# Kernel optimization log

Measured on AMD Instinct MI355X. Metric: run time of the kernel, lower is better.

## Reference

```python
import jax, jax.numpy as jnp
import numpy as np

B, T, IN, H = 4096, 128, 768, 256


def setup_inputs() -> dict:
    key = jax.random.key(0)
    ks = jax.random.split(key, 5)
    s1 = 1.0 / np.sqrt(IN)
    s2 = 1.0 / np.sqrt(H)
    return {
        "x": jax.random.normal(ks[0], (B, IN), jnp.float32),
        "W1": jax.random.normal(ks[1], (T, IN, H), jnp.float32) * s1,
        "b1": jnp.zeros((T, H), jnp.float32),
        "W2": jax.random.normal(ks[2], (T, H, H), jnp.float32) * s2,
        "b2": jnp.zeros((T, H), jnp.float32),
        "W3": jax.random.normal(ks[3], (T, H), jnp.float32) * s2,
        "b3": jnp.zeros((T,), jnp.float32),
    }


def reference(x, W1, b1, W2, b2, W3, b3):
    # Per-task 3-layer MLP, vectorized over tasks. Dropout is eval-mode (identity).
    h = jax.nn.relu(jnp.einsum('bi,tih->bth', x, W1) + b1)          # [B, T, H]
    h = jax.nn.relu(jnp.einsum('bth,thk->btk', h, W2) + b2)         # [B, T, H]
    out = jnp.einsum('bth,th->bt', h, W3) + b3                      # [B, T]
    return out
```

## Files before the change

kernel.cpp:

```cpp
#include <hip/hip_runtime.h>
#include <cstdint>
#include <cstddef>

#define B_   4096
#define T_   128
#define IN_  768
#define H_   256
#define BM_  256
#define KC1  (IN_ / 32)
#define KC2  (H_ / 32)

typedef __bf16 bf16_t;
typedef bf16_t bf16x8 __attribute__((ext_vector_type(8)));
typedef bf16_t bf16x4 __attribute__((ext_vector_type(4)));
typedef float  floatx16 __attribute__((ext_vector_type(16)));

#define MFMA32(a, b, c) __builtin_amdgcn_mfma_f32_32x32x16_bf16((a), (b), (c), 0, 0, 0)

__device__ __forceinline__ void gl_lds16(const bf16_t* g, bf16_t* l) {
    __builtin_amdgcn_global_load_lds(
        (const __attribute__((address_space(1))) void*)g,
        (__attribute__((address_space(3))) void*)l, 16, 0, 0);
}

__global__ __launch_bounds__(256)
void tile_w2(const float* __restrict__ src, bf16_t* __restrict__ dst, int K, int KC) {
    const int t  = blockIdx.x / KC;
    const int kc = blockIdx.x - t * KC;
    const int kq = threadIdx.x >> 6;
    const int h4 = (threadIdx.x & 63) * 4;
    const float* s = src + ((size_t)t * K + kc * 32 + kq * 8) * H_ + h4;
    float r[8][4];
#pragma unroll
    for (int e = 0; e < 8; ++e) {
        float4 v = *(const float4*)(s + (size_t)e * H_);
        r[e][0] = v.x; r[e][1] = v.y; r[e][2] = v.z; r[e][3] = v.w;
    }
    bf16_t* d = dst + (((size_t)(t * KC + kc) * 4 + kq) * H_ + h4) * 8;
#pragma unroll
    for (int c = 0; c < 4; ++c) {
        bf16x8 v;
#pragma unroll
        for (int e = 0; e < 8; ++e) v[e] = (bf16_t)r[e][c];
        *(bf16x8*)(d + c * 8) = v;
    }
}

__global__ void tile_x_kernel(const float* __restrict__ src, bf16_t* __restrict__ dst,
                              long long total8) {
    long long o = (long long)blockIdx.x * blockDim.x + threadIdx.x;
    if (o >= total8) return;
    int m = (int)(o & 127);
    long long q = o >> 7;
    int kq = (int)(q & 3);
    int q2 = (int)(q >> 2);
    int kc   = q2 % KC1;
    int mblk = q2 / KC1;
    const float* s = src + ((long long)mblk * 128 + m) * IN_ + kc * 32 + kq * 8;
    float4 a = *(const float4*)s;
    float4 b = *(const float4*)(s + 4);
    bf16x8 v;
    v[0] = (bf16_t)a.x; v[1] = (bf16_t)a.y; v[2] = (bf16_t)a.z; v[3] = (bf16_t)a.w;
    v[4] = (bf16_t)b.x; v[5] = (bf16_t)b.y; v[6] = (bf16_t)b.z; v[7] = (bf16_t)b.w;
    *(bf16x8*)(dst + o * 8) = v;
}

__global__ __launch_bounds__(512, 2)
void mtmlp_fused3(const bf16_t* __restrict__ xt, const bf16_t* __restrict__ w1t,
                  const float* __restrict__ b1, const bf16_t* __restrict__ w2t,
                  const float* __restrict__ b2, const float* __restrict__ W3,
                  const float* __restrict__ b3, float* __restrict__ out) {
    const int L    = blockIdx.x;
    const int xcd  = L & 7;
    const int slot = L >> 3;
    const int t    = xcd * 16 + (slot >> 4);
    const int mblk = slot & 15;
    const int m0   = mblk * BM_;
    const int mb0  = mblk * 2;

    const int tid  = threadIdx.x;
    const int lane = tid & 63;
    const int wid  = tid >> 6;
    const int wm   = wid >> 2;
    const int wn   = wid & 3;
    const int ln31 = lane & 31;
    const int hi   = lane >> 5;

    __shared__ __align__(16) bf16_t hbuf[BM_ * H_];
    __shared__ __align__(16) bf16_t wt2[4 * H_ * 8];
    float* w3s = (float*)wt2;

    floatx16 acc[4][2];
#pragma unroll
    for (int i = 0; i < 4; ++i)
#pragma unroll
        for (int j = 0; j < 2; ++j)
#pragma unroll
            for (int e = 0; e < 16; ++e) acc[i][j][e] = 0.0f;

    const bf16_t* w1base = w1t + (size_t)t * KC1 * 8192;
    const bf16_t* x0base = xt + (size_t)mb0 * KC1 * 4096;
    const bf16_t* x1base = xt + (size_t)(mb0 + 1) * KC1 * 4096;

    auto stage1 = [&](bf16_t* buf, int kc) {
        const bf16_t* ws = w1base + (size_t)kc * 8192;
        gl_lds16(ws + tid * 8,        buf + tid * 8);
        gl_lds16(ws + 4096 + tid * 8, buf + 4096 + tid * 8);
        gl_lds16(x0base + (size_t)kc * 4096 + tid * 8, buf + 8192 + tid * 8);
        gl_lds16(x1base + (size_t)kc * 4096 + tid * 8, buf + 12288 + tid * 8);
    };
    auto comp1 = [&](const bf16_t* buf) {
#pragma unroll
        for (int s = 0; s < 2; ++s) {
            const int kq = s * 2 + hi;
            bf16x8 A[4], Bf[2];
#pragma unroll
            for (int i = 0; i < 4; ++i)
                A[i] = *(const bf16x8*)(buf + (size_t)(kq * H_ + wm * 128 + i * 32 + ln31) * 8);
#pragma unroll
            for (int j = 0; j < 2; ++j) {
                const int mm = wn * 64 + j * 32 + ln31;
                Bf[j] = *(const bf16x8*)(buf + 8192 + (mm >> 7) * 4096 +
                                         (size_t)(kq * 128 + (mm & 127)) * 8);
            }
#pragma unroll
            for (int i = 0; i < 4; ++i)
#pragma unroll
                for (int j = 0; j < 2; ++j) acc[i][j] = MFMA32(A[i], Bf[j], acc[i][j]);
        }
    };

    bf16_t* buf0 = hbuf;
    bf16_t* buf1 = hbuf + 16384;
    stage1(buf0, 0);
    for (int kc = 0; kc < KC1; kc += 2) {
        __syncthreads();
        stage1(buf1, kc + 1);
        comp1(buf0);
        __syncthreads();
        if (kc + 2 < KC1) stage1(buf0, kc + 2);
        comp1(buf1);
    }
    __syncthreads();

#pragma unroll
    for (int i = 0; i < 4; ++i) {
#pragma unroll
        for (int g = 0; g < 4; ++g) {
            const int h0 = wm * 128 + i * 32 + g * 8 + 4 * hi;
            float4 bias = *(const float4*)(b1 + t * H_ + h0);
            const int blk = h0 >> 3;
#pragma unroll
            for (int j = 0; j < 2; ++j) {
                const int mm = wn * 64 + j * 32 + ln31;
                bf16x4 o;
                o[0] = (bf16_t)fmaxf(acc[i][j][4 * g + 0] + bias.x, 0.0f);
                o[1] = (bf16_t)fmaxf(acc[i][j][4 * g + 1] + bias.y, 0.0f);
                o[2] = (bf16_t)fmaxf(acc[i][j][4 * g + 2] + bias.z, 0.0f);
                o[3] = (bf16_t)fmaxf(acc[i][j][4 * g + 3] + bias.w, 0.0f);
                *(bf16x4*)(hbuf + (size_t)(blk * BM_ + mm) * 8 + 4 * hi) = o;
            }
        }
    }

#pragma unroll
    for (int i = 0; i < 4; ++i)
#pragma unroll
        for (int j = 0; j < 2; ++j)
#pragma unroll
            for (int e = 0; e < 16; ++e) acc[i][j][e] = 0.0f;

    const bf16_t* w2base = w2t + (size_t)t * KC2 * 8192;
    for (int kc = 0; kc < KC2; ++kc) {
        __syncthreads();
        const bf16_t* ws = w2base + (size_t)kc * 8192;
        gl_lds16(ws + tid * 8,        wt2 + tid * 8);
        gl_lds16(ws + 4096 + tid * 8, wt2 + 4096 + tid * 8);
        __syncthreads();
#pragma unroll
        for (int s = 0; s < 2; ++s) {
            const int kq = s * 2 + hi;
            bf16x8 A[4], Bf[2];
#pragma unroll
            for (int i = 0; i < 4; ++i)
                A[i] = *(const bf16x8*)(wt2 + (size_t)(kq * H_ + wm * 128 + i * 32 + ln31) * 8);
            const int blk = kc * 4 + kq;
#pragma unroll
            for (int j = 0; j < 2; ++j) {
                const int mm = wn * 64 + j * 32 + ln31;
                Bf[j] = *(const bf16x8*)(hbuf + (size_t)(blk * BM_ + mm) * 8);
            }
#pragma unroll
            for (int i = 0; i < 4; ++i)
#pragma unroll
                for (int j = 0; j < 2; ++j) acc[i][j] = MFMA32(A[i], Bf[j], acc[i][j]);
        }
    }

    __syncthreads();
    if (tid < H_) w3s[tid] = W3[t * H_ + tid];
#pragma unroll
    for (int i = 0; i < 4; ++i) {
#pragma unroll
        for (int g = 0; g < 4; ++g) {
            const int h0 = wm * 128 + i * 32 + g * 8 + 4 * hi;
            float4 bias = *(const float4*)(b2 + t * H_ + h0);
            const int blk = h0 >> 3;
#pragma unroll
            for (int j = 0; j < 2; ++j) {
                const int mm = wn * 64 + j * 32 + ln31;
                bf16x4 o;
                o[0] = (bf16_t)fmaxf(acc[i][j][4 * g + 0] + bias.x, 0.0f);
                o[1] = (bf16_t)fmaxf(acc[i][j][4 * g + 1] + bias.y, 0.0f);
                o[2] = (bf16_t)fmaxf(acc[i][j][4 * g + 2] + bias.z, 0.0f);
                o[3] = (bf16_t)fmaxf(acc[i][j][4 * g + 3] + bias.w, 0.0f);
                *(bf16x4*)(hbuf + (size_t)(blk * BM_ + mm) * 8 + 4 * hi) = o;
            }
        }
    }
    __syncthreads();

    {
        const int m = tid >> 1, seg = tid & 1;
        float sum = 0.0f;
#pragma unroll
        for (int b = 0; b < 16; ++b) {
            const int blk = seg * 16 + b;
            const bf16x8 v = *(const bf16x8*)(hbuf + (size_t)(blk * BM_ + m) * 8);
            const float* w = w3s + blk * 8;
#pragma unroll
            for (int e = 0; e < 8; ++e) sum += (float)v[e] * w[e];
        }
        sum += __shfl_xor(sum, 1);
        if (seg == 0) out[(size_t)(m0 + m) * T_ + t] = sum + b3[t];
    }
}

extern "C" void kernel_launch(void* const* d_in, const int* in_sizes, int n_in,
                              void* d_out, int out_size, void* d_ws, size_t ws_size,
                              hipStream_t stream) {
    const float* x  = (const float*)d_in[0];
    const float* W1 = (const float*)d_in[1];
    const float* b1 = (const float*)d_in[2];
    const float* W2 = (const float*)d_in[3];
    const float* b2 = (const float*)d_in[4];
    const float* W3 = (const float*)d_in[5];
    const float* b3 = (const float*)d_in[6];
    float* out = (float*)d_out;

    const size_t nx  = (size_t)B_ * IN_;
    const size_t nw1 = (size_t)T_ * IN_ * H_;
    const size_t nw2 = (size_t)T_ * H_ * H_;

    bf16_t* xt  = (bf16_t*)d_ws;
    bf16_t* w1t = xt + nx;
    bf16_t* w2t = w1t + nw1;

    tile_x_kernel<<<dim3((unsigned)(nx / 8 / 256)), 256, 0, stream>>>(x, xt, (long long)(nx / 8));
    tile_w2<<<dim3(T_ * KC1), 256, 0, stream>>>(W1, w1t, IN_, KC1);
    tile_w2<<<dim3(T_ * KC2), 256, 0, stream>>>(W2, w2t, H_, KC2);

    mtmlp_fused3<<<dim3(2048), 512, 0, stream>>>(xt, w1t, b1, w2t, b2, W3, b3, out);
}
```

Baseline: 474.4 us.

## Deepen load pipelines with vmcnt waits and merge tiling kernels into one launch

Replaces the double-buffered layer-1 loop with a 4-slot ring. Each stage now waits on a partial s_waitcnt vmcnt and a raw s_barrier instead of full __syncthreads, so several async global-to-LDS loads stay in flight. Layer 2 gets a 3-slot ring of smaller W2 chunks whose prefetch starts while the layer-1 epilogue runs. The three preprocessing kernels become one launch, with a new x-tiling path that reads coalesced rows. Launch bounds drop to one block per SM, and correctness now depends on the hand-counted vmcnt values.

```diff
diff --git a/kernel.cpp b/kernel.cpp
--- a/kernel.cpp
+++ b/kernel.cpp
@@ -8,7 +8,7 @@
 #define H_   256
 #define BM_  256
 #define KC1  (IN_ / 32)
-#define KC2  (H_ / 32)
+#define NC2  16
 
 typedef __bf16 bf16_t;
 typedef bf16_t bf16x8 __attribute__((ext_vector_type(8)));
@@ -23,50 +23,58 @@
         (__attribute__((address_space(3))) void*)l, 16, 0, 0);
 }
 
+template <int N>
+__device__ __forceinline__ void vmwait() {
+    asm volatile("s_waitcnt vmcnt(%0)" :: "i"(N) : "memory");
+}
+__device__ __forceinline__ void wg_barrier() {
+    asm volatile("" ::: "memory");
+    __builtin_amdgcn_s_barrier();
+    asm volatile("" ::: "memory");
+}
+
 __global__ __launch_bounds__(256)
-void tile_w2(const float* __restrict__ src, bf16_t* __restrict__ dst, int K, int KC) {
-    const int t  = blockIdx.x / KC;
-    const int kc = blockIdx.x - t * KC;
-    const int kq = threadIdx.x >> 6;
-    const int h4 = (threadIdx.x & 63) * 4;
-    const float* s = src + ((size_t)t * K + kc * 32 + kq * 8) * H_ + h4;
-    float r[8][4];
-#pragma unroll
-    for (int e = 0; e < 8; ++e) {
-        float4 v = *(const float4*)(s + (size_t)e * H_);
-        r[e][0] = v.x; r[e][1] = v.y; r[e][2] = v.z; r[e][3] = v.w;
-    }
-    bf16_t* d = dst + (((size_t)(t * KC + kc) * 4 + kq) * H_ + h4) * 8;
-#pragma unroll
-    for (int c = 0; c < 4; ++c) {
-        bf16x8 v;
-#pragma unroll
-        for (int e = 0; e < 8; ++e) v[e] = (bf16_t)r[e][c];
-        *(bf16x8*)(d + c * 8) = v;
-    }
-}
-
-__global__ void tile_x_kernel(const float* __restrict__ src, bf16_t* __restrict__ dst,
-                              long long total8) {
-    long long o = (long long)blockIdx.x * blockDim.x + threadIdx.x;
-    if (o >= total8) return;
-    int m = (int)(o & 127);
-    long long q = o >> 7;
-    int kq = (int)(q & 3);
-    int q2 = (int)(q >> 2);
-    int kc   = q2 % KC1;
-    int mblk = q2 / KC1;
-    const float* s = src + ((long long)mblk * 128 + m) * IN_ + kc * 32 + kq * 8;
-    float4 a = *(const float4*)s;
-    float4 b = *(const float4*)(s + 4);
-    bf16x8 v;
-    v[0] = (bf16_t)a.x; v[1] = (bf16_t)a.y; v[2] = (bf16_t)a.z; v[3] = (bf16_t)a.w;
-    v[4] = (bf16_t)b.x; v[5] = (bf16_t)b.y; v[6] = (bf16_t)b.z; v[7] = (bf16_t)b.w;
-    *(bf16x8*)(dst + o * 8) = v;
-}
-
-__global__ __launch_bounds__(512, 2)
-void mtmlp_fused3(const bf16_t* __restrict__ xt, const bf16_t* __restrict__ w1t,
+void tile_all(const float* __restrict__ x, const float* __restrict__ W1,
+              const float* __restrict__ W2, bf16_t* __restrict__ xt,
+              bf16_t* __restrict__ w1t, bf16_t* __restrict__ w2t) {
+    const int b   = blockIdx.x;
+    const int tid = threadIdx.x;
+    if (b < T_ * KC1 + T_ * 8) {
+        const float* src; bf16_t* dst; int t, kc, K, KC;
+        if (b < T_ * KC1) { t = b / KC1; kc = b - t * KC1; K = IN_; KC = KC1; src = W1; dst = w1t; }
+        else { int bb = b - T_ * KC1; t = bb >> 3; kc = bb & 7; K = H_; KC = 8; src = W2; dst = w2t; }
+        const int kq = tid >> 6, h4 = (tid & 63) * 4;
+        const float* s = src + ((size_t)t * K + kc * 32 + kq * 8) * H_ + h4;
+        float r[8][4];
+#pragma unroll
+        for (int e = 0; e < 8; ++e) {
+            float4 v = *(const float4*)(s + (size_t)e * H_);
+            r[e][0] = v.x; r[e][1] = v.y; r[e][2] = v.z; r[e][3] = v.w;
+        }
+        bf16_t* d = dst + (((size_t)(t * KC + kc) * 4 + kq) * H_ + h4) * 8;
+#pragma unroll
+        for (int c = 0; c < 4; ++c) {
+            bf16x8 v;
+#pragma unroll
+            for (int e = 0; e < 8; ++e) v[e] = (bf16_t)r[e][c];
+            *(bf16x8*)(d + c * 8) = v;
+        }
+    } else {
+        const int bb = b - (T_ * KC1 + T_ * 8);
+        const int mb = bb / KC1, kc = bb - mb * KC1;
+        const int r = tid >> 3, c = tid & 7;
+#pragma unroll
+        for (int it = 0; it < 4; ++it) {
+            const int m = it * 32 + r;
+            float4 v = *(const float4*)(x + ((size_t)(mb * 128 + m)) * IN_ + kc * 32 + c * 4);
+            bf16x4 o; o[0] = (bf16_t)v.x; o[1] = (bf16_t)v.y; o[2] = (bf16_t)v.z; o[3] = (bf16_t)v.w;
+            *(bf16x4*)(xt + ((size_t)(mb * KC1 + kc) * 4 + (c >> 1)) * 1024 + m * 8 + (c & 1) * 4) = o;
+        }
+    }
+}
+
+__global__ __launch_bounds__(512, 1)
+void mtmlp_fused5(const bf16_t* __restrict__ xt, const bf16_t* __restrict__ w1t,
                   const float* __restrict__ b1, const bf16_t* __restrict__ w2t,
                   const float* __restrict__ b2, const float* __restrict__ W3,
                   const float* __restrict__ b3, float* __restrict__ out) {
@@ -87,7 +95,7 @@
     const int hi   = lane >> 5;
 
     __shared__ __align__(16) bf16_t hbuf[BM_ * H_];
-    __shared__ __align__(16) bf16_t wt2[4 * H_ * 8];
+    __shared__ __align__(16) bf16_t wt2[3 * 4096];
     float* w3s = (float*)wt2;
 
     floatx16 acc[4][2];
@@ -102,14 +110,16 @@
     const bf16_t* x0base = xt + (size_t)mb0 * KC1 * 4096;
     const bf16_t* x1base = xt + (size_t)(mb0 + 1) * KC1 * 4096;
 
-    auto stage1 = [&](bf16_t* buf, int kc) {
+    auto stage1 = [&](int sl, int kc) {
+        bf16_t* buf = hbuf + sl * 16384;
         const bf16_t* ws = w1base + (size_t)kc * 8192;
         gl_lds16(ws + tid * 8,        buf + tid * 8);
         gl_lds16(ws + 4096 + tid * 8, buf + 4096 + tid * 8);
         gl_lds16(x0base + (size_t)kc * 4096 + tid * 8, buf + 8192 + tid * 8);
         gl_lds16(x1base + (size_t)kc * 4096 + tid * 8, buf + 12288 + tid * 8);
     };
-    auto comp1 = [&](const bf16_t* buf) {
+    auto comp1 = [&](int sl) {
+        const bf16_t* buf = hbuf + sl * 16384;
 #pragma unroll
         for (int s = 0; s < 2; ++s) {
             const int kq = s * 2 + hi;
@@ -130,18 +140,24 @@
         }
     };
 
-    bf16_t* buf0 = hbuf;
-    bf16_t* buf1 = hbuf + 16384;
-    stage1(buf0, 0);
-    for (int kc = 0; kc < KC1; kc += 2) {
-        __syncthreads();
-        stage1(buf1, kc + 1);
-        comp1(buf0);
-        __syncthreads();
-        if (kc + 2 < KC1) stage1(buf0, kc + 2);
-        comp1(buf1);
-    }
-    __syncthreads();
+    stage1(0, 0); stage1(1, 1); stage1(2, 2);
+    for (int kc = 0; kc <= KC1 - 4; ++kc) {
+        vmwait<8>();
+        wg_barrier();
+        stage1((kc + 3) & 3, kc + 3);
+        comp1(kc & 3);
+    }
+    vmwait<8>(); wg_barrier(); comp1((KC1 - 3) & 3);
+    vmwait<4>(); wg_barrier(); comp1((KC1 - 2) & 3);
+    vmwait<0>(); wg_barrier(); comp1((KC1 - 1) & 3);
+
+    __syncthreads();
+
+    const bf16_t* w2base = w2t + (size_t)t * 32 * 2048;
+    auto stage2 = [&](int sl, int c) {
+        gl_lds16(w2base + (size_t)c * 4096 + tid * 8, wt2 + sl * 4096 + tid * 8);
+    };
+    stage2(0, 0); stage2(1, 1);
 
 #pragma unroll
     for (int i = 0; i < 4; ++i) {
@@ -170,34 +186,42 @@
 #pragma unroll
             for (int e = 0; e < 16; ++e) acc[i][j][e] = 0.0f;
 
-    const bf16_t* w2base = w2t + (size_t)t * KC2 * 8192;
-    for (int kc = 0; kc < KC2; ++kc) {
-        __syncthreads();
-        const bf16_t* ws = w2base + (size_t)kc * 8192;
-        gl_lds16(ws + tid * 8,        wt2 + tid * 8);
-        gl_lds16(ws + 4096 + tid * 8, wt2 + 4096 + tid * 8);
-        __syncthreads();
-#pragma unroll
-        for (int s = 0; s < 2; ++s) {
-            const int kq = s * 2 + hi;
-            bf16x8 A[4], Bf[2];
-#pragma unroll
-            for (int i = 0; i < 4; ++i)
-                A[i] = *(const bf16x8*)(wt2 + (size_t)(kq * H_ + wm * 128 + i * 32 + ln31) * 8);
-            const int blk = kc * 4 + kq;
-#pragma unroll
-            for (int j = 0; j < 2; ++j) {
-                const int mm = wn * 64 + j * 32 + ln31;
-                Bf[j] = *(const bf16x8*)(hbuf + (size_t)(blk * BM_ + mm) * 8);
-            }
-#pragma unroll
-            for (int i = 0; i < 4; ++i)
-#pragma unroll
-                for (int j = 0; j < 2; ++j) acc[i][j] = MFMA32(A[i], Bf[j], acc[i][j]);
-        }
-    }
-
-    __syncthreads();
+    __syncthreads();
+
+    auto comp2 = [&](int sl, int c) {
+        const bf16_t* buf = wt2 + sl * 4096;
+        bf16x8 A[4], Bf[2];
+#pragma unroll
+        for (int i = 0; i < 4; ++i)
+            A[i] = *(const bf16x8*)(buf + (size_t)(hi * H_ + wm * 128 + i * 32 + ln31) * 8);
+        const int blk = c * 2 + hi;
+#pragma unroll
+        for (int j = 0; j < 2; ++j) {
+            const int mm = wn * 64 + j * 32 + ln31;
+            Bf[j] = *(const bf16x8*)(hbuf + (size_t)(blk * BM_ + mm) * 8);
+        }
+#pragma unroll
+        for (int i = 0; i < 4; ++i)
+#pragma unroll
+            for (int j = 0; j < 2; ++j) acc[i][j] = MFMA32(A[i], Bf[j], acc[i][j]);
+    };
+
+    {
+        int sl = 0, sp = 2;
+        for (int c = 0; c <= NC2 - 3; ++c) {
+            vmwait<1>();
+            wg_barrier();
+            stage2(sp, c + 2);
+            comp2(sl, c);
+            sl = (sl == 2) ? 0 : sl + 1;
+            sp = (sp == 2) ? 0 : sp + 1;
+        }
+    }
+    vmwait<1>(); wg_barrier(); comp2((NC2 - 2) % 3, NC2 - 2);
+    vmwait<0>(); wg_barrier(); comp2((NC2 - 1) % 3, NC2 - 1);
+
+    __syncthreads();
+
     if (tid < H_) w3s[tid] = W3[t * H_ + tid];
 #pragma unroll
     for (int i = 0; i < 4; ++i) {
@@ -250,15 +274,11 @@
 
     const size_t nx  = (size_t)B_ * IN_;
     const size_t nw1 = (size_t)T_ * IN_ * H_;
-    const size_t nw2 = (size_t)T_ * H_ * H_;
 
     bf16_t* xt  = (bf16_t*)d_ws;
     bf16_t* w1t = xt + nx;
     bf16_t* w2t = w1t + nw1;
 
-    tile_x_kernel<<<dim3((unsigned)(nx / 8 / 256)), 256, 0, stream>>>(x, xt, (long long)(nx / 8));
-    tile_w2<<<dim3(T_ * KC1), 256, 0, stream>>>(W1, w1t, IN_, KC1);
-    tile_w2<<<dim3(T_ * KC2), 256, 0, stream>>>(W2, w2t, H_, KC2);
-
-    mtmlp_fused3<<<dim3(2048), 512, 0, stream>>>(xt, w1t, b1, w2t, b2, W3, b3, out);
-}
+    tile_all<<<dim3(T_ * KC1 + T_ * 8 + 32 * KC1), 256, 0, stream>>>(x, W1, W2, xt, w1t, w2t);
+    mtmlp_fused5<<<dim3(2048), 512, 0, stream>>>(xt, w1t, b1, w2t, b2, W3, b3, out);
+}
```

Result: slower. 485.7 us (+2.4%).
